# Kernel tuning notes

Hardware: AMD Instinct MI355X
Metric: run time of the kernel (lower is better)

The kernel has to match this reference:

```python
import jax, jax.numpy as jnp
import numpy as np

B, NQ, C, H, W, HEADS = 8, 300, 256, 64, 64, 8
HD = C // HEADS
SCALING = float(HD) ** (-0.5)


def setup_inputs() -> dict:
    key = jax.random.key(0)
    ks = jax.random.split(key, 12)
    pts = jax.random.uniform(ks[3], (B, NQ, 2), jnp.float32)
    pts = pts * jnp.array([W - 1, H - 1], jnp.float32)  # (x, y) in pixel coords
    s = 1.0 / np.sqrt(C)
    return {
        "query": jax.random.normal(ks[0], (B, NQ, C), jnp.float32),
        "key": jax.random.normal(ks[1], (B, C, H, W), jnp.float32),
        "value": jax.random.normal(ks[2], (B, C, H, W), jnp.float32),
        "sampling_points": pts,
        "Wq": jax.random.normal(ks[4], (C, C), jnp.float32) * s,
        "bq": jnp.zeros((C,), jnp.float32),
        "Wk": jax.random.normal(ks[5], (C, C), jnp.float32) * s,
        "bk": jnp.zeros((C,), jnp.float32),
        "Wv": jax.random.normal(ks[6], (C, C), jnp.float32) * s,
        "bv": jnp.zeros((C,), jnp.float32),
        "Wo": jax.random.normal(ks[7], (C, C), jnp.float32) * s,
        "bo": jnp.zeros((C,), jnp.float32),
    }


def _sample_rows(feat, y):
    # feat: [b,heads,hd,h,w]; y: [b,q] float row coordinate.
    # Returns feat linearly interpolated in y for every column: [b,q,heads,hd,w]
    h = feat.shape[3]
    y0f = jnp.clip(jnp.floor(y), 0.0, h - 1)
    wy = y - y0f
    y0 = y0f.astype(jnp.int32)
    y1 = jnp.clip(y0 + 1, 0, h - 1)
    g = jax.vmap(lambda f, idx: f[:, :, idx, :])  # per-batch -> [heads,hd,q,w]
    r = g(feat, y0) * (1.0 - wy)[:, None, None, :, None] + g(feat, y1) * wy[:, None, None, :, None]
    return jnp.transpose(r, (0, 3, 1, 2, 4))


def _sample_cols(feat, x):
    # feat: [b,heads,hd,h,w]; x: [b,q] float col coordinate -> [b,q,heads,hd,h]
    w = feat.shape[4]
    x0f = jnp.clip(jnp.floor(x), 0.0, w - 1)
    wx = x - x0f
    x0 = x0f.astype(jnp.int32)
    x1 = jnp.clip(x0 + 1, 0, w - 1)
    g = jax.vmap(lambda f, idx: f[:, :, :, idx])  # per-batch -> [heads,hd,h,q]
    c = g(feat, x0) * (1.0 - wx)[:, None, None, None, :] + g(feat, x1) * wx[:, None, None, None, :]
    return jnp.transpose(c, (0, 4, 1, 2, 3))


def reference(query, key, value, sampling_points, Wq, bq, Wk, bk, Wv, bv, Wo, bo):
    b, nq, c = query.shape
    h, w = key.shape[2], key.shape[3]
    pq = (query @ Wq.T + bq) * SCALING                     # [b,nq,C]
    pk = jnp.einsum('oc,bchw->bohw', Wk, key) + bk[None, :, None, None]
    pv = jnp.einsum('oc,bchw->bohw', Wv, value) + bv[None, :, None, None]
    pq = pq.reshape(b, nq, HEADS, HD)
    pk = pk.reshape(b, HEADS, HD, h, w)
    pv = pv.reshape(b, HEADS, HD, h, w)
    x, y = sampling_points[..., 0], sampling_points[..., 1]
    # criss-cross weights: row through y (w samples) + column through x (h samples)
    k_row = _sample_rows(pk, y)                            # [b,q,heads,hd,w]
    k_col = _sample_cols(pk, x)                            # [b,q,heads,hd,h]
    w_row = jnp.einsum('bqnd,bqndw->bqnw', pq, k_row)
    w_col = jnp.einsum('bqnd,bqndk->bqnk', pq, k_col)
    attn = jax.nn.softmax(jnp.concatenate([w_row, w_col], axis=-1), axis=-1)
    a_row, a_col = attn[..., :w], attn[..., w:]
    v_row = _sample_rows(pv, y)
    v_col = _sample_cols(pv, x)
    out = jnp.einsum('bqnw,bqndw->bqnd', a_row, v_row) + jnp.einsum('bqnk,bqndk->bqnd', a_col, v_col)
    out = out.reshape(b, nq, c)
    return out @ Wo.T + bo
```

## Files before the change

kernel.cpp:

```cpp
#include <hip/hip_runtime.h>
#include <hip/hip_bf16.h>
#include <math.h>

constexpr int cB = 8, cNQ = 300, cC = 256, cH = 64, cW = 64, cHEADS = 8, cHD = 32;
constexpr int cHW = cH * cW;
constexpr int cM = cB * cNQ;
constexpr float cSCALE = 0.1767766952966369f;

typedef __bf16 bf16_t;
typedef bf16_t bf16x4 __attribute__((ext_vector_type(4)));
typedef bf16_t bf16x8 __attribute__((ext_vector_type(8)));
typedef float f32x4 __attribute__((ext_vector_type(4)));
typedef _Float16 f16_t;
typedef f16_t f16x2 __attribute__((ext_vector_type(2)));
typedef f16_t f16x8 __attribute__((ext_vector_type(8)));

__device__ __forceinline__ float dot2acc(f16x2 a, f16x2 b, float c) {
#if __has_builtin(__builtin_amdgcn_fdot2)
  return __builtin_amdgcn_fdot2(a, b, c, false);
#else
  return c + (float)a.x * (float)b.x + (float)a.y * (float)b.y;
#endif
}

__global__ __launch_bounds__(256) void proj_mfma_k(
    const float* __restrict__ X, const float* __restrict__ Wt,
    const float* __restrict__ bias, float* __restrict__ out,
    float scale, int M) {
  __shared__ bf16_t Xs[128 * 64];
  __shared__ bf16_t Ws[64 * 64];
  int m0 = blockIdx.x * 128;
  int o0 = blockIdx.y * 64;
  int tid = threadIdx.x;
  int lane = tid & 63, w = tid >> 6;
  int moff = (w & 1) * 64, ooff = (w >> 1) * 32;
  int l15 = lane & 15, l4 = lane >> 4;
  int srow = tid >> 1;
  int schalf = (tid & 1) * 32;
  int wo_l = tid >> 2;
  int wcg = (tid & 3) * 16;

  f32x4 acc[4][2];
#pragma unroll
  for (int m = 0; m < 4; ++m)
#pragma unroll
    for (int n = 0; n < 2; ++n) acc[m][n] = (f32x4){0.f, 0.f, 0.f, 0.f};

  for (int c0 = 0; c0 < cC; c0 += 64) {
    {
      int mrow = min(m0 + srow, M - 1);
      const float4* xr = (const float4*)(X + (size_t)mrow * cC + c0 + schalf);
      int sw = (srow & 7) * 8;
#pragma unroll
      for (int i = 0; i < 4; ++i) {
        float4 a = xr[i * 2], b4 = xr[i * 2 + 1];
        bf16x8 v = {(bf16_t)a.x, (bf16_t)a.y, (bf16_t)a.z, (bf16_t)a.w,
                    (bf16_t)b4.x, (bf16_t)b4.y, (bf16_t)b4.z, (bf16_t)b4.w};
        *(bf16x8*)&Xs[srow * 64 + ((schalf + i * 8) ^ sw)] = v;
      }
    }
    {
      const float4* wr = (const float4*)(Wt + (size_t)(o0 + wo_l) * cC + c0 + wcg);
      float4 a = wr[0], b4 = wr[1], c4 = wr[2], d4 = wr[3];
      bf16x8 w0 = {(bf16_t)a.x, (bf16_t)a.y, (bf16_t)a.z, (bf16_t)a.w,
                   (bf16_t)b4.x, (bf16_t)b4.y, (bf16_t)b4.z, (bf16_t)b4.w};
      bf16x8 w1 = {(bf16_t)c4.x, (bf16_t)c4.y, (bf16_t)c4.z, (bf16_t)c4.w,
                   (bf16_t)d4.x, (bf16_t)d4.y, (bf16_t)d4.z, (bf16_t)d4.w};
      int sw = (wo_l & 7) * 8;
      *(bf16x8*)&Ws[wo_l * 64 + (wcg ^ sw)] = w0;
      *(bf16x8*)&Ws[wo_l * 64 + ((wcg + 8) ^ sw)] = w1;
    }
    __syncthreads();
#pragma unroll
    for (int s = 0; s < 2; ++s) {
      int c8 = s * 32 + l4 * 8;
      bf16x8 afr[4], bfr[2];
#pragma unroll
      for (int m = 0; m < 4; ++m) {
        int r = moff + m * 16 + l15;
        afr[m] = *(const bf16x8*)&Xs[r * 64 + (c8 ^ ((r & 7) * 8))];
      }
#pragma unroll
      for (int n = 0; n < 2; ++n) {
        int r = ooff + n * 16 + l15;
        bfr[n] = *(const bf16x8*)&Ws[r * 64 + (c8 ^ ((r & 7) * 8))];
      }
#pragma unroll
      for (int m = 0; m < 4; ++m)
#pragma unroll
        for (int n = 0; n < 2; ++n)
          acc[m][n] = __builtin_amdgcn_mfma_f32_16x16x32_bf16(
              afr[m], bfr[n], acc[m][n], 0, 0, 0);
    }
    __syncthreads();
  }

  float b0 = bias[o0 + ooff + l15];
  float b1 = bias[o0 + ooff + 16 + l15];
#pragma unroll
  for (int m = 0; m < 4; ++m) {
    int mr = m0 + moff + m * 16 + l4 * 4;
#pragma unroll
    for (int reg = 0; reg < 4; ++reg) {
      if (mr + reg < M) {
        out[(size_t)(mr + reg) * cC + o0 + ooff + l15] =
            (acc[m][0][reg] + b0) * scale;
        out[(size_t)(mr + reg) * cC + o0 + ooff + 16 + l15] =
            (acc[m][1][reg] + b1) * scale;
      }
    }
  }
}

__global__ __launch_bounds__(512) void unified_proj_k(
    const float* __restrict__ key, const float* __restrict__ value,
    const float* __restrict__ query,
    const float* __restrict__ Wk, const float* __restrict__ bk,
    const float* __restrict__ Wv, const float* __restrict__ bv,
    const float* __restrict__ Wq, const float* __restrict__ bq,
    f16_t* __restrict__ pkT, f16_t* __restrict__ pvT,
    f16_t* __restrict__ pqh) {
  __shared__ bf16_t Xs[128 * 64];
  __shared__ bf16_t Wf[16 * 64 * 8];

  int z = blockIdx.z;
  int tid = threadIdx.x;
  int lane = tid & 63, w = tid >> 6;
  int l15 = lane & 15, l4 = lane >> 4;
  int wo_l = tid >> 2;
  int wcg = (tid & 3) * 16;
  int wks = wcg >> 5;
  int wl4 = (wcg & 31) >> 3;
  int wnt = wo_l >> 4, wl15 = wo_l & 15;
  int hwoff = (w >> 2) * 64;
  int nb = (w & 3) * 2;

  f32x4 acc[4][2];
#pragma unroll
  for (int m = 0; m < 4; ++m)
#pragma unroll
    for (int n = 0; n < 2; ++n) acc[m][n] = (f32x4){0.f, 0.f, 0.f, 0.f};

  if (z < 16) {
    int b = z >> 1;
    bool isv = z & 1;
    const float* X = (isv ? value : key) + (size_t)b * cC * cHW;
    const float* Wm = isv ? Wv : Wk;
    const float* bb = isv ? bv : bk;
    f16_t* outT = (isv ? pvT : pkT) + (size_t)b * cHEADS * cHW * cHD;
    int hw0 = blockIdx.x * 128;
    int o0 = blockIdx.y * 128;

    int cq = tid & 15;
    int hwg = tid >> 4;
    const float* xbase = X + hw0 + hwg * 4;
    const float* wbase = Wm + (size_t)(o0 + wo_l) * cC + wcg;

    float4 xr4[4];
    float4 wr[4];
    auto issue = [&](int c0) {
#pragma unroll
      for (int i = 0; i < 4; ++i)
        xr4[i] = *(const float4*)(xbase + (size_t)(c0 + cq * 4 + i) * cHW);
      const float4* p = (const float4*)(wbase + c0);
      wr[0] = p[0]; wr[1] = p[1]; wr[2] = p[2]; wr[3] = p[3];
    };

    issue(0);
#pragma unroll
    for (int s = 0; s < 4; ++s) {
#pragma unroll
      for (int j = 0; j < 4; ++j) {
        int row = hwg * 4 + j;
        bf16x4 v = {(bf16_t)xr4[0][j], (bf16_t)xr4[1][j],
                    (bf16_t)xr4[2][j], (bf16_t)xr4[3][j]};
        *(bf16x4*)&Xs[row * 64 + ((cq * 4) ^ ((row & 7) * 8))] = v;
      }
      {
        bf16x8 v0 = {(bf16_t)wr[0].x, (bf16_t)wr[0].y, (bf16_t)wr[0].z, (bf16_t)wr[0].w,
                     (bf16_t)wr[1].x, (bf16_t)wr[1].y, (bf16_t)wr[1].z, (bf16_t)wr[1].w};
        bf16x8 v1 = {(bf16_t)wr[2].x, (bf16_t)wr[2].y, (bf16_t)wr[2].z, (bf16_t)wr[2].w,
                     (bf16_t)wr[3].x, (bf16_t)wr[3].y, (bf16_t)wr[3].z, (bf16_t)wr[3].w};
        *(bf16x8*)&Wf[(size_t)((wks * 8 + wnt) * 64 + wl4 * 16 + wl15) * 8] = v0;
        *(bf16x8*)&Wf[(size_t)((wks * 8 + wnt) * 64 + (wl4 + 1) * 16 + wl15) * 8] = v1;
      }
      if (s < 3) issue((s + 1) * 64);
      __syncthreads();
#pragma unroll
      for (int ks = 0; ks < 2; ++ks) {
        int c8 = ks * 32 + l4 * 8;
        bf16x8 bf0 = *(const bf16x8*)&Wf[(size_t)((ks * 8 + nb) * 64 + lane) * 8];
        bf16x8 bf1 = *(const bf16x8*)&Wf[(size_t)((ks * 8 + nb + 1) * 64 + lane) * 8];
#pragma unroll
        for (int m = 0; m < 4; ++m) {
          int r = hwoff + m * 16 + l15;
          bf16x8 a = *(const bf16x8*)&Xs[r * 64 + (c8 ^ ((r & 7) * 8))];
          acc[m][0] = __builtin_amdgcn_mfma_f32_16x16x32_bf16(a, bf0, acc[m][0], 0, 0, 0);
          acc[m][1] = __builtin_amdgcn_mfma_f32_16x16x32_bf16(a, bf1, acc[m][1], 0, 0, 0);
        }
      }
      if (s < 3) __syncthreads();
    }

    int osub = o0 + nb * 16;
    int head = osub >> 5;
    f16_t* obase = outT + (size_t)head * cHW * cHD;
    float bias0 = bb[osub + l15];
    float bias1 = bb[osub + 16 + l15];
#pragma unroll
    for (int m = 0; m < 4; ++m) {
      int hwr = hwoff + m * 16 + l4 * 4;
#pragma unroll
      for (int reg = 0; reg < 4; ++reg) {
        int hw = hw0 + hwr + reg;
        size_t rowoff = (size_t)hw * cHD;
        obase[rowoff + l15] = (f16_t)(acc[m][0][reg] + bias0);
        obase[rowoff + 16 + l15] = (f16_t)(acc[m][1][reg] + bias1);
      }
    }
  } else {
    if (blockIdx.x >= (cM + 127) / 128) return;
    int m0 = blockIdx.x * 128;
    int o0 = blockIdx.y * 128;

    int srow = tid >> 2;
    int scg = (tid & 3) * 16;
    const float* wbase = Wq + (size_t)(o0 + wo_l) * cC + wcg;

    float4 xa[4], wr[4];
    auto issue = [&](int c0) {
      int mrow = min(m0 + srow, cM - 1);
      const float4* xr = (const float4*)(query + (size_t)mrow * cC + c0 + scg);
      xa[0] = xr[0]; xa[1] = xr[1]; xa[2] = xr[2]; xa[3] = xr[3];
      const float4* p = (const float4*)(wbase + c0);
      wr[0] = p[0]; wr[1] = p[1]; wr[2] = p[2]; wr[3] = p[3];
    };

    issue(0);
#pragma unroll
    for (int s = 0; s < 4; ++s) {
      {
        int sw = (srow & 7) * 8;
        bf16x8 v0 = {(bf16_t)xa[0].x, (bf16_t)xa[0].y, (bf16_t)xa[0].z, (bf16_t)xa[0].w,
                     (bf16_t)xa[1].x, (bf16_t)xa[1].y, (bf16_t)xa[1].z, (bf16_t)xa[1].w};
        bf16x8 v1 = {(bf16_t)xa[2].x, (bf16_t)xa[2].y, (bf16_t)xa[2].z, (bf16_t)xa[2].w,
                     (bf16_t)xa[3].x, (bf16_t)xa[3].y, (bf16_t)xa[3].z, (bf16_t)xa[3].w};
        *(bf16x8*)&Xs[srow * 64 + (scg ^ sw)] = v0;
        *(bf16x8*)&Xs[srow * 64 + ((scg + 8) ^ sw)] = v1;
      }
      {
        bf16x8 v0 = {(bf16_t)wr[0].x, (bf16_t)wr[0].y, (bf16_t)wr[0].z, (bf16_t)wr[0].w,
                     (bf16_t)wr[1].x, (bf16_t)wr[1].y, (bf16_t)wr[1].z, (bf16_t)wr[1].w};
        bf16x8 v1 = {(bf16_t)wr[2].x, (bf16_t)wr[2].y, (bf16_t)wr[2].z, (bf16_t)wr[2].w,
                     (bf16_t)wr[3].x, (bf16_t)wr[3].y, (bf16_t)wr[3].z, (bf16_t)wr[3].w};
        *(bf16x8*)&Wf[(size_t)((wks * 8 + wnt) * 64 + wl4 * 16 + wl15) * 8] = v0;
        *(bf16x8*)&Wf[(size_t)((wks * 8 + wnt) * 64 + (wl4 + 1) * 16 + wl15) * 8] = v1;
      }
      if (s < 3) issue((s + 1) * 64);
      __syncthreads();
#pragma unroll
      for (int ks = 0; ks < 2; ++ks) {
        int c8 = ks * 32 + l4 * 8;
        bf16x8 bf0 = *(const bf16x8*)&Wf[(size_t)((ks * 8 + nb) * 64 + lane) * 8];
        bf16x8 bf1 = *(const bf16x8*)&Wf[(size_t)((ks * 8 + nb + 1) * 64 + lane) * 8];
#pragma unroll
        for (int m = 0; m < 4; ++m) {
          int r = hwoff + m * 16 + l15;
          bf16x8 a = *(const bf16x8*)&Xs[r * 64 + (c8 ^ ((r & 7) * 8))];
          acc[m][0] = __builtin_amdgcn_mfma_f32_16x16x32_bf16(a, bf0, acc[m][0], 0, 0, 0);
          acc[m][1] = __builtin_amdgcn_mfma_f32_16x16x32_bf16(a, bf1, acc[m][1], 0, 0, 0);
        }
      }
      if (s < 3) __syncthreads();
    }

    int osub = o0 + nb * 16;
    float bias0 = bq[osub + l15];
    float bias1 = bq[osub + 16 + l15];
#pragma unroll
    for (int m = 0; m < 4; ++m) {
      int mr = m0 + hwoff + m * 16 + l4 * 4;
#pragma unroll
      for (int reg = 0; reg < 4; ++reg) {
        if (mr + reg < cM) {
          pqh[(size_t)(mr + reg) * cC + osub + l15] =
              (f16_t)((acc[m][0][reg] + bias0) * cSCALE);
          pqh[(size_t)(mr + reg) * cC + osub + 16 + l15] =
              (f16_t)((acc[m][1][reg] + bias1) * cSCALE);
        }
      }
    }
  }
}

__global__ __launch_bounds__(256) void attn_k(
    const f16_t* __restrict__ pqh, const f16_t* __restrict__ pkT,
    const f16_t* __restrict__ pvT, const float* __restrict__ pts,
    float* __restrict__ out) {
  int bid = blockIdx.x;
  int xcd = bid & 7;
  int t = bid >> 3;
  int phase = (t >= cNQ) ? 1 : 0;
  int q = t - phase * cNQ;
  int g = xcd + 8 * phase;
  int b = g >> 1;
  int pair = g & 1;
  int lane = threadIdx.x & 63;
  int wid = threadIdx.x >> 6;
  int n = pair * 4 + wid;

  float x = pts[((size_t)b * cNQ + q) * 2 + 0];
  float y = pts[((size_t)b * cNQ + q) * 2 + 1];
  float y0f = fminf(fmaxf(floorf(y), 0.f), (float)(cH - 1));
  float x0f = fminf(fmaxf(floorf(x), 0.f), (float)(cW - 1));
  float wy = y - y0f, wx = x - x0f;
  int y0 = (int)y0f, y1 = min(y0 + 1, cH - 1);
  int x0 = (int)x0f, x1 = min(x0 + 1, cW - 1);

  size_t hoff = (size_t)(b * cHEADS + n) * cHW * cHD;
  const f16_t* kTb = pkT + hoff;
  const f16_t* vTb = pvT + hoff;

  int g16 = lane >> 2, ch = lane & 3;

  f16x8 qv = *(const f16x8*)(pqh + ((size_t)b * cNQ + q) * cC + n * cHD + ch * 8);
  const f16x2* qp = (const f16x2*)&qv;

  float wrowA[4], wcolA[4];
#pragma unroll
  for (int k = 0; k < 4; ++k) {
    int p = g16 * 4 + k;
    f16x8 a0 = *(const f16x8*)(kTb + (size_t)(y0 * cW + p) * cHD + ch * 8);
    f16x8 a1 = *(const f16x8*)(kTb + (size_t)(y1 * cW + p) * cHD + ch * 8);
    f16x8 b0 = *(const f16x8*)(kTb + (size_t)(p * cW + x0) * cHD + ch * 8);
    f16x8 b1 = *(const f16x8*)(kTb + (size_t)(p * cW + x1) * cHD + ch * 8);
    const f16x2* a0p = (const f16x2*)&a0;
    const f16x2* a1p = (const f16x2*)&a1;
    const f16x2* b0p = (const f16x2*)&b0;
    const f16x2* b1p = (const f16x2*)&b1;
    float s0 = 0.f, s1 = 0.f, t0 = 0.f, t1 = 0.f;
#pragma unroll
    for (int j2 = 0; j2 < 4; ++j2) {
      f16x2 qq = qp[j2];
      s0 = dot2acc(a0p[j2], qq, s0);
      s1 = dot2acc(a1p[j2], qq, s1);
      t0 = dot2acc(b0p[j2], qq, t0);
      t1 = dot2acc(b1p[j2], qq, t1);
    }
    float wrow = s0 + wy * (s1 - s0);
    float wcol = t0 + wx * (t1 - t0);
    wrow += __shfl_xor(wrow, 1, 64);
    wrow += __shfl_xor(wrow, 2, 64);
    wcol += __shfl_xor(wcol, 1, 64);
    wcol += __shfl_xor(wcol, 2, 64);
    wrowA[k] = wrow;
    wcolA[k] = wcol;
  }

  float m = -1e30f;
#pragma unroll
  for (int k = 0; k < 4; ++k) m = fmaxf(m, fmaxf(wrowA[k], wcolA[k]));
#pragma unroll
  for (int sh = 4; sh <= 32; sh <<= 1) m = fmaxf(m, __shfl_xor(m, sh, 64));
  float er[4], ec[4];
  float ssl = 0.f;
#pragma unroll
  for (int k = 0; k < 4; ++k) {
    er[k] = __expf(wrowA[k] - m);
    ec[k] = __expf(wcolA[k] - m);
    ssl += er[k] + ec[k];
  }
  float ssum = ssl;
#pragma unroll
  for (int sh = 4; sh <= 32; sh <<= 1) ssum += __shfl_xor(ssum, sh, 64);

  float omwy = 1.f - wy, omwx = 1.f - wx;
  float acc[8];
#pragma unroll
  for (int j = 0; j < 8; ++j) acc[j] = 0.f;
#pragma unroll
  for (int k = 0; k < 4; ++k) {
    int p = g16 * 4 + k;
    f16x8 r0 = *(const f16x8*)(vTb + (size_t)(y0 * cW + p) * cHD + ch * 8);
    f16x8 r1 = *(const f16x8*)(vTb + (size_t)(y1 * cW + p) * cHD + ch * 8);
    f16x8 c0 = *(const f16x8*)(vTb + (size_t)(p * cW + x0) * cHD + ch * 8);
    f16x8 c1 = *(const f16x8*)(vTb + (size_t)(p * cW + x1) * cHD + ch * 8);
    float wr0 = er[k] * omwy, wr1 = er[k] * wy;
    float wc0 = ec[k] * omwx, wc1 = ec[k] * wx;
#pragma unroll
    for (int j = 0; j < 8; ++j) {
      acc[j] += wr0 * (float)r0[j] + wr1 * (float)r1[j] +
                wc0 * (float)c0[j] + wc1 * (float)c1[j];
    }
  }
#pragma unroll
  for (int sh = 4; sh <= 32; sh <<= 1)
#pragma unroll
    for (int j = 0; j < 8; ++j) acc[j] += __shfl_xor(acc[j], sh, 64);

  float inv = 1.f / ssum;
  if (lane < 4) {
    float* op = out + ((size_t)b * cNQ + q) * cC + n * cHD + ch * 8;
    float4 o0 = {acc[0] * inv, acc[1] * inv, acc[2] * inv, acc[3] * inv};
    float4 o1 = {acc[4] * inv, acc[5] * inv, acc[6] * inv, acc[7] * inv};
    *(float4*)op = o0;
    *(float4*)(op + 4) = o1;
  }
}

extern "C" void kernel_launch(void* const* d_in, const int* in_sizes, int n_in,
                              void* d_out, int out_size, void* d_ws, size_t ws_size,
                              hipStream_t stream) {
  const float* query = (const float*)d_in[0];
  const float* key   = (const float*)d_in[1];
  const float* value = (const float*)d_in[2];
  const float* pts   = (const float*)d_in[3];
  const float* Wq = (const float*)d_in[4];
  const float* bq = (const float*)d_in[5];
  const float* Wk = (const float*)d_in[6];
  const float* bk = (const float*)d_in[7];
  const float* Wv = (const float*)d_in[8];
  const float* bv = (const float*)d_in[9];
  const float* Wo = (const float*)d_in[10];
  const float* bo = (const float*)d_in[11];
  float* out = (float*)d_out;

  const size_t kvsz = (size_t)cB * cC * cHW;
  f16_t* pqh = (f16_t*)d_ws;
  f16_t* pkT = pqh + (size_t)cM * cC;
  f16_t* pvT = pkT + kvsz;
  float* ao = (float*)(pvT + kvsz);

  unified_proj_k<<<dim3(32, 2, 17), 512, 0, stream>>>(
      key, value, query, Wk, bk, Wv, bv, Wq, bq, pkT, pvT, pqh);
  attn_k<<<cB * cNQ * 2, 256, 0, stream>>>(pqh, pkT, pvT, pts, ao);
  proj_mfma_k<<<dim3((cM + 127) / 128, cC / 64), 256, 0, stream>>>(
      ao, Wo, bo, out, 1.0f, cM);
}
```

Before: 87.99 us.

## Shrink projection tiles to 128x64 with 256-thread blocks for more blocks

The unified K/V/Q projection kernel moves from 512-thread blocks computing 128x128 output tiles to 256-thread blocks computing 128x64 tiles, doubling the grid's y dimension. The goal is more blocks, better CU occupancy and less LDS per block. The query branch loses its register-prefetch pipeline and becomes a simple load-sync-compute loop with a swizzled row-major weight layout in LDS. In exchange the key/value input tiles are reloaded for every output tile, which doubles that global read traffic, and the query path can no longer overlap its loads with compute.

```diff
diff --git a/kernel.cpp b/kernel.cpp
--- a/kernel.cpp
+++ b/kernel.cpp
@@ -112,7 +112,7 @@
   }
 }
 
-__global__ __launch_bounds__(512) void unified_proj_k(
+__global__ __launch_bounds__(256) void unified_proj_k(
     const float* __restrict__ key, const float* __restrict__ value,
     const float* __restrict__ query,
     const float* __restrict__ Wk, const float* __restrict__ bk,
@@ -121,19 +121,16 @@
     f16_t* __restrict__ pkT, f16_t* __restrict__ pvT,
     f16_t* __restrict__ pqh) {
   __shared__ bf16_t Xs[128 * 64];
-  __shared__ bf16_t Wf[16 * 64 * 8];
+  __shared__ bf16_t Wsh[64 * 64];
 
   int z = blockIdx.z;
   int tid = threadIdx.x;
   int lane = tid & 63, w = tid >> 6;
   int l15 = lane & 15, l4 = lane >> 4;
+  int moff = (w & 1) * 64;
+  int nb2 = (w >> 1) * 2;
   int wo_l = tid >> 2;
   int wcg = (tid & 3) * 16;
-  int wks = wcg >> 5;
-  int wl4 = (wcg & 31) >> 3;
-  int wnt = wo_l >> 4, wl15 = wo_l & 15;
-  int hwoff = (w >> 2) * 64;
-  int nb = (w & 3) * 2;
 
   f32x4 acc[4][2];
 #pragma unroll
@@ -149,19 +146,27 @@
     const float* bb = isv ? bv : bk;
     f16_t* outT = (isv ? pvT : pkT) + (size_t)b * cHEADS * cHW * cHD;
     int hw0 = blockIdx.x * 128;
-    int o0 = blockIdx.y * 128;
+    int o0 = blockIdx.y * 64;
+
+    int wks = wcg >> 5;
+    int wl4 = (wcg & 31) >> 3;
+    int wnt = wo_l >> 4, wl15 = wo_l & 15;
 
     int cq = tid & 15;
     int hwg = tid >> 4;
-    const float* xbase = X + hw0 + hwg * 4;
+    const float* xbase = X + hw0 + hwg * 8;
     const float* wbase = Wm + (size_t)(o0 + wo_l) * cC + wcg;
 
-    float4 xr4[4];
+    float xf[4][8];
     float4 wr[4];
     auto issue = [&](int c0) {
 #pragma unroll
-      for (int i = 0; i < 4; ++i)
-        xr4[i] = *(const float4*)(xbase + (size_t)(c0 + cq * 4 + i) * cHW);
+      for (int i = 0; i < 4; ++i) {
+        const float4* p = (const float4*)(xbase + (size_t)(c0 + cq * 4 + i) * cHW);
+        float4 t0 = p[0], t1 = p[1];
+        xf[i][0] = t0.x; xf[i][1] = t0.y; xf[i][2] = t0.z; xf[i][3] = t0.w;
+        xf[i][4] = t1.x; xf[i][5] = t1.y; xf[i][6] = t1.z; xf[i][7] = t1.w;
+      }
       const float4* p = (const float4*)(wbase + c0);
       wr[0] = p[0]; wr[1] = p[1]; wr[2] = p[2]; wr[3] = p[3];
     };
@@ -170,10 +175,10 @@
 #pragma unroll
     for (int s = 0; s < 4; ++s) {
 #pragma unroll
-      for (int j = 0; j < 4; ++j) {
-        int row = hwg * 4 + j;
-        bf16x4 v = {(bf16_t)xr4[0][j], (bf16_t)xr4[1][j],
-                    (bf16_t)xr4[2][j], (bf16_t)xr4[3][j]};
+      for (int j = 0; j < 8; ++j) {
+        int row = hwg * 8 + j;
+        bf16x4 v = {(bf16_t)xf[0][j], (bf16_t)xf[1][j],
+                    (bf16_t)xf[2][j], (bf16_t)xf[3][j]};
         *(bf16x4*)&Xs[row * 64 + ((cq * 4) ^ ((row & 7) * 8))] = v;
       }
       {
@@ -181,19 +186,19 @@
                      (bf16_t)wr[1].x, (bf16_t)wr[1].y, (bf16_t)wr[1].z, (bf16_t)wr[1].w};
         bf16x8 v1 = {(bf16_t)wr[2].x, (bf16_t)wr[2].y, (bf16_t)wr[2].z, (bf16_t)wr[2].w,
                      (bf16_t)wr[3].x, (bf16_t)wr[3].y, (bf16_t)wr[3].z, (bf16_t)wr[3].w};
-        *(bf16x8*)&Wf[(size_t)((wks * 8 + wnt) * 64 + wl4 * 16 + wl15) * 8] = v0;
-        *(bf16x8*)&Wf[(size_t)((wks * 8 + wnt) * 64 + (wl4 + 1) * 16 + wl15) * 8] = v1;
+        *(bf16x8*)&Wsh[(size_t)((wks * 4 + wnt) * 64 + wl4 * 16 + wl15) * 8] = v0;
+        *(bf16x8*)&Wsh[(size_t)((wks * 4 + wnt) * 64 + (wl4 + 1) * 16 + wl15) * 8] = v1;
       }
       if (s < 3) issue((s + 1) * 64);
       __syncthreads();
 #pragma unroll
       for (int ks = 0; ks < 2; ++ks) {
         int c8 = ks * 32 + l4 * 8;
-        bf16x8 bf0 = *(const bf16x8*)&Wf[(size_t)((ks * 8 + nb) * 64 + lane) * 8];
-        bf16x8 bf1 = *(const bf16x8*)&Wf[(size_t)((ks * 8 + nb + 1) * 64 + lane) * 8];
+        bf16x8 bf0 = *(const bf16x8*)&Wsh[(size_t)((ks * 4 + nb2) * 64 + lane) * 8];
+        bf16x8 bf1 = *(const bf16x8*)&Wsh[(size_t)((ks * 4 + nb2 + 1) * 64 + lane) * 8];
 #pragma unroll
         for (int m = 0; m < 4; ++m) {
-          int r = hwoff + m * 16 + l15;
+          int r = moff + m * 16 + l15;
           bf16x8 a = *(const bf16x8*)&Xs[r * 64 + (c8 ^ ((r & 7) * 8))];
           acc[m][0] = __builtin_amdgcn_mfma_f32_16x16x32_bf16(a, bf0, acc[m][0], 0, 0, 0);
           acc[m][1] = __builtin_amdgcn_mfma_f32_16x16x32_bf16(a, bf1, acc[m][1], 0, 0, 0);
@@ -202,14 +207,14 @@
       if (s < 3) __syncthreads();
     }
 
-    int osub = o0 + nb * 16;
+    int osub = o0 + nb2 * 16;
     int head = osub >> 5;
     f16_t* obase = outT + (size_t)head * cHW * cHD;
     float bias0 = bb[osub + l15];
     float bias1 = bb[osub + 16 + l15];
 #pragma unroll
     for (int m = 0; m < 4; ++m) {
-      int hwr = hwoff + m * 16 + l4 * 4;
+      int hwr = moff + m * 16 + l4 * 4;
 #pragma unroll
       for (int reg = 0; reg < 4; ++reg) {
         int hw = hw0 + hwr + reg;
@@ -221,72 +226,73 @@
   } else {
     if (blockIdx.x >= (cM + 127) / 128) return;
     int m0 = blockIdx.x * 128;
-    int o0 = blockIdx.y * 128;
-
-    int srow = tid >> 2;
-    int scg = (tid & 3) * 16;
-    const float* wbase = Wq + (size_t)(o0 + wo_l) * cC + wcg;
-
-    float4 xa[4], wr[4];
-    auto issue = [&](int c0) {
-      int mrow = min(m0 + srow, cM - 1);
-      const float4* xr = (const float4*)(query + (size_t)mrow * cC + c0 + scg);
-      xa[0] = xr[0]; xa[1] = xr[1]; xa[2] = xr[2]; xa[3] = xr[3];
-      const float4* p = (const float4*)(wbase + c0);
-      wr[0] = p[0]; wr[1] = p[1]; wr[2] = p[2]; wr[3] = p[3];
-    };
-
-    issue(0);
-#pragma unroll
-    for (int s = 0; s < 4; ++s) {
+    int o0 = blockIdx.y * 64;
+    int ooff = nb2 * 16;
+
+    int srow = tid >> 1;
+    int schalf = (tid & 1) * 32;
+
+    for (int c0 = 0; c0 < cC; c0 += 64) {
       {
+        int mrow = min(m0 + srow, cM - 1);
+        const float4* xr = (const float4*)(query + (size_t)mrow * cC + c0 + schalf);
         int sw = (srow & 7) * 8;
-        bf16x8 v0 = {(bf16_t)xa[0].x, (bf16_t)xa[0].y, (bf16_t)xa[0].z, (bf16_t)xa[0].w,
-                     (bf16_t)xa[1].x, (bf16_t)xa[1].y, (bf16_t)xa[1].z, (bf16_t)xa[1].w};
-        bf16x8 v1 = {(bf16_t)xa[2].x, (bf16_t)xa[2].y, (bf16_t)xa[2].z, (bf16_t)xa[2].w,
-                     (bf16_t)xa[3].x, (bf16_t)xa[3].y, (bf16_t)xa[3].z, (bf16_t)xa[3].w};
-        *(bf16x8*)&Xs[srow * 64 + (scg ^ sw)] = v0;
-        *(bf16x8*)&Xs[srow * 64 + ((scg + 8) ^ sw)] = v1;
+#pragma unroll
+        for (int i = 0; i < 4; ++i) {
+          float4 a = xr[i * 2], b4 = xr[i * 2 + 1];
+          bf16x8 v = {(bf16_t)a.x, (bf16_t)a.y, (bf16_t)a.z, (bf16_t)a.w,
+                      (bf16_t)b4.x, (bf16_t)b4.y, (bf16_t)b4.z, (bf16_t)b4.w};
+          *(bf16x8*)&Xs[srow * 64 + ((schalf + i * 8) ^ sw)] = v;
+        }
       }
       {
-        bf16x8 v0 = {(bf16_t)wr[0].x, (bf16_t)wr[0].y, (bf16_t)wr[0].z, (bf16_t)wr[0].w,
-                     (bf16_t)wr[1].x, (bf16_t)wr[1].y, (bf16_t)wr[1].z, (bf16_t)wr[1].w};
-        bf16x8 v1 = {(bf16_t)wr[2].x, (bf16_t)wr[2].y, (bf16_t)wr[2].z, (bf16_t)wr[2].w,
-                     (bf16_t)wr[3].x, (bf16_t)wr[3].y, (bf16_t)wr[3].z, (bf16_t)wr[3].w};
-        *(bf16x8*)&Wf[(size_t)((wks * 8 + wnt) * 64 + wl4 * 16 + wl15) * 8] = v0;
-        *(bf16x8*)&Wf[(size_t)((wks * 8 + wnt) * 64 + (wl4 + 1) * 16 + wl15) * 8] = v1;
-      }
-      if (s < 3) issue((s + 1) * 64);
+        const float4* wrp = (const float4*)(Wq + (size_t)(o0 + wo_l) * cC + c0 + wcg);
+        float4 a = wrp[0], b4 = wrp[1], c4 = wrp[2], d4 = wrp[3];
+        bf16x8 w0 = {(bf16_t)a.x, (bf16_t)a.y, (bf16_t)a.z, (bf16_t)a.w,
+                     (bf16_t)b4.x, (bf16_t)b4.y, (bf16_t)b4.z, (bf16_t)b4.w};
+        bf16x8 w1 = {(bf16_t)c4.x, (bf16_t)c4.y, (bf16_t)c4.z, (bf16_t)c4.w,
+                     (bf16_t)d4.x, (bf16_t)d4.y, (bf16_t)d4.z, (bf16_t)d4.w};
+        int sw = (wo_l & 7) * 8;
+        *(bf16x8*)&Wsh[wo_l * 64 + (wcg ^ sw)] = w0;
+        *(bf16x8*)&Wsh[wo_l * 64 + ((wcg + 8) ^ sw)] = w1;
+      }
       __syncthreads();
 #pragma unroll
-      for (int ks = 0; ks < 2; ++ks) {
-        int c8 = ks * 32 + l4 * 8;
-        bf16x8 bf0 = *(const bf16x8*)&Wf[(size_t)((ks * 8 + nb) * 64 + lane) * 8];
-        bf16x8 bf1 = *(const bf16x8*)&Wf[(size_t)((ks * 8 + nb + 1) * 64 + lane) * 8];
+      for (int s = 0; s < 2; ++s) {
+        int c8 = s * 32 + l4 * 8;
+        bf16x8 afr[4], bfr[2];
 #pragma unroll
         for (int m = 0; m < 4; ++m) {
-          int r = hwoff + m * 16 + l15;
-          bf16x8 a = *(const bf16x8*)&Xs[r * 64 + (c8 ^ ((r & 7) * 8))];
-          acc[m][0] = __builtin_amdgcn_mfma_f32_16x16x32_bf16(a, bf0, acc[m][0], 0, 0, 0);
-          acc[m][1] = __builtin_amdgcn_mfma_f32_16x16x32_bf16(a, bf1, acc[m][1], 0, 0, 0);
+          int r = moff + m * 16 + l15;
+          afr[m] = *(const bf16x8*)&Xs[r * 64 + (c8 ^ ((r & 7) * 8))];
         }
-      }
-      if (s < 3) __syncthreads();
-    }
-
-    int osub = o0 + nb * 16;
-    float bias0 = bq[osub + l15];
-    float bias1 = bq[osub + 16 + l15];
+#pragma unroll
+        for (int n = 0; n < 2; ++n) {
+          int r = ooff + n * 16 + l15;
+          bfr[n] = *(const bf16x8*)&Wsh[r * 64 + (c8 ^ ((r & 7) * 8))];
+        }
+#pragma unroll
+        for (int m = 0; m < 4; ++m)
+#pragma unroll
+          for (int n = 0; n < 2; ++n)
+            acc[m][n] = __builtin_amdgcn_mfma_f32_16x16x32_bf16(
+                afr[m], bfr[n], acc[m][n], 0, 0, 0);
+      }
+      __syncthreads();
+    }
+
+    float b0 = bq[o0 + ooff + l15];
+    float b1 = bq[o0 + ooff + 16 + l15];
 #pragma unroll
     for (int m = 0; m < 4; ++m) {
-      int mr = m0 + hwoff + m * 16 + l4 * 4;
+      int mr = m0 + moff + m * 16 + l4 * 4;
 #pragma unroll
       for (int reg = 0; reg < 4; ++reg) {
         if (mr + reg < cM) {
-          pqh[(size_t)(mr + reg) * cC + osub + l15] =
-              (f16_t)((acc[m][0][reg] + bias0) * cSCALE);
-          pqh[(size_t)(mr + reg) * cC + osub + 16 + l15] =
-              (f16_t)((acc[m][1][reg] + bias1) * cSCALE);
+          pqh[(size_t)(mr + reg) * cC + o0 + ooff + l15] =
+              (f16_t)((acc[m][0][reg] + b0) * cSCALE);
+          pqh[(size_t)(mr + reg) * cC + o0 + ooff + 16 + l15] =
+              (f16_t)((acc[m][1][reg] + b1) * cSCALE);
         }
       }
     }
@@ -431,7 +437,7 @@
   f16_t* pvT = pkT + kvsz;
   float* ao = (float*)(pvT + kvsz);
 
-  unified_proj_k<<<dim3(32, 2, 17), 512, 0, stream>>>(
+  unified_proj_k<<<dim3(32, 4, 17), 256, 0, stream>>>(
       key, value, query, Wk, bk, Wv, bv, Wq, bq, pkT, pvT, pqh);
   attn_k<<<cB * cNQ * 2, 256, 0, stream>>>(pqh, pkT, pvT, pts, ao);
   proj_mfma_k<<<dim3((cM + 127) / 128, cC / 64), 256, 0, stream>>>(
```

Measured after the change: 101.0 us. 14.8% more time.
